# Kernel optimization log

Measured on AMD Instinct MI355X. Metric: run time of the kernel, lower is better.

The kernel has to match this reference:

```python
import jax, jax.numpy as jnp
import numpy as np

N_HEAD = 16


def _rope_cache(T, head_dim):
    half = head_dim // 2
    inv_freq = 1.0 / (10000.0 ** (jnp.arange(half, dtype=jnp.float32) / half))
    t = jnp.arange(T, dtype=jnp.float32)
    freqs = jnp.einsum('i,j->ij', t, inv_freq)            # (T, half)
    cos = jnp.repeat(jnp.cos(freqs), 2, axis=-1)          # (T, head_dim)
    sin = jnp.repeat(jnp.sin(freqs), 2, axis=-1)
    return cos, sin


def _apply_rope(x, cos, sin):
    # x: (B, H, T, D); cos/sin: (T, D)
    x1 = x[..., ::2]
    x2 = x[..., 1::2]
    x_rot = jnp.stack([-x2, x1], axis=-1).reshape(x.shape)
    return x * cos[None, None] + x_rot * sin[None, None]


def setup_inputs() -> dict:
    key = jax.random.key(0)
    k1, k2, k3 = jax.random.split(key, 3)
    B, T, C = 2, 2048, 1024
    x = jax.random.normal(k1, (B, T, C), dtype=jnp.float32)
    Wqkv = jax.random.normal(k2, (C, 3 * C), dtype=jnp.float32) * 0.02
    Wo = jax.random.normal(k3, (C, C), dtype=jnp.float32) * 0.02
    bo = jnp.zeros((C,), dtype=jnp.float32)
    return {"x": x, "Wqkv": Wqkv, "Wo": Wo, "bo": bo}


def reference(x, Wqkv, Wo, bo):
    B, T, C = x.shape
    H = N_HEAD
    D = C // H
    scale = D ** -0.5

    qkv = x @ Wqkv                                        # (B, T, 3C)
    qkv = qkv.reshape(B, T, 3, H, D).transpose(2, 0, 3, 1, 4)  # (3, B, H, T, D)
    q, k, v = qkv[0], qkv[1], qkv[2]

    cos, sin = _rope_cache(T, D)
    q = _apply_rope(q, cos, sin)
    k = _apply_rope(k, cos, sin)

    att = jnp.einsum('bhqd,bhkd->bhqk', q, k) * scale     # (B, H, T, T)
    causal = jnp.tril(jnp.ones((T, T), dtype=bool))
    att = jnp.where(causal[None, None], att, -jnp.inf)
    att = jax.nn.softmax(att, axis=-1)                    # dropout is identity in eval

    out = jnp.einsum('bhqk,bhkd->bhqd', att, v)           # (B, H, T, D)
    out = out.transpose(0, 2, 1, 3).reshape(B, T, C)
    return out @ Wo + bo
```

## Files before the change

### kernel.cpp

```cpp
#include <hip/hip_runtime.h>

typedef __attribute__((ext_vector_type(8))) short bf16x8;
typedef __attribute__((ext_vector_type(4))) float f32x4;
typedef __attribute__((ext_vector_type(4))) unsigned uint32x4;

#define MFMA32(a, b, c) __builtin_amdgcn_mfma_f32_16x16x32_bf16((a), (b), (c), 0, 0, 0)

__device__ __forceinline__ unsigned short f2bf(float f) {
  unsigned u = __builtin_bit_cast(unsigned, f);
  u += 0x7fffu + ((u >> 16) & 1u);
  return (unsigned short)(u >> 16);
}
__device__ __forceinline__ unsigned pack2(float a, float b) {
  return (unsigned)f2bf(a) | ((unsigned)f2bf(b) << 16);
}
__device__ __forceinline__ unsigned pack2t(float lo, float hi) {
  return __builtin_amdgcn_perm(__builtin_bit_cast(unsigned, hi),
                               __builtin_bit_cast(unsigned, lo), 0x07060302u);
}
__device__ __forceinline__ void gl_lds16(const unsigned short* g, unsigned short* l) {
  __builtin_amdgcn_global_load_lds(
      (const __attribute__((address_space(1))) unsigned int*)(g),
      (__attribute__((address_space(3))) unsigned int*)(l), 16, 0, 0);
}

#define QSCALE 0.18033688011112042f

__global__ __launch_bounds__(256) void prep_kernel(
    const float* __restrict__ x, const float* __restrict__ Wqkv,
    const float* __restrict__ Wo, unsigned short* __restrict__ xb,
    unsigned short* __restrict__ wqt, unsigned short* __restrict__ wot) {
  __shared__ unsigned short Tl[64][72];
  const int bid = blockIdx.x, tid = threadIdx.x;
  if (bid < 2048) {
    int i = (bid * 256 + tid) * 8;
    float4 a = *(const float4*)(x + i);
    float4 b = *(const float4*)(x + i + 4);
    uint4 w;
    w.x = pack2(a.x, a.y); w.y = pack2(a.z, a.w);
    w.z = pack2(b.x, b.y); w.w = pack2(b.z, b.w);
    *(uint4*)(xb + i) = w;
  } else {
    const float* src;
    unsigned short* dst;
    int N, kt, nt;
    if (bid < 2816) {
      int r = bid - 2048;
      src = Wqkv; dst = wqt; N = 3072;
      nt = (r % 48) * 64; kt = (r / 48) * 64;
    } else {
      int r = bid - 2816;
      src = Wo; dst = wot; N = 1024;
      nt = (r & 15) * 64; kt = (r >> 4) * 64;
    }
    const int rr = tid >> 2, cs = (tid & 3) * 16;
    const float* sp = src + (kt + rr) * N + nt + cs;
    uint4 w0, w1;
    {
      float4 a = *(const float4*)(sp), b = *(const float4*)(sp + 4);
      float4 c = *(const float4*)(sp + 8), d = *(const float4*)(sp + 12);
      w0.x = pack2(a.x, a.y); w0.y = pack2(a.z, a.w);
      w0.z = pack2(b.x, b.y); w0.w = pack2(b.z, b.w);
      w1.x = pack2(c.x, c.y); w1.y = pack2(c.z, c.w);
      w1.z = pack2(d.x, d.y); w1.w = pack2(d.z, d.w);
    }
    *(uint4*)(&Tl[rr][cs]) = w0;
    *(uint4*)(&Tl[rr][cs + 8]) = w1;
    __syncthreads();
    unsigned short tmp[16];
#pragma unroll
    for (int i = 0; i < 16; i++) tmp[i] = Tl[cs + i][rr];
    unsigned short* dp = dst + (nt + rr) * 1024 + kt + cs;
    *(uint4*)(dp) = *(const uint4*)(&tmp[0]);
    *(uint4*)(dp + 8) = *(const uint4*)(&tmp[8]);
  }
}

__global__ __launch_bounds__(256, 6) void qkv_rope_kernel(
    const unsigned short* __restrict__ xb, const unsigned short* __restrict__ wt,
    unsigned short* __restrict__ qws, unsigned short* __restrict__ kws,
    unsigned short* __restrict__ vws) {
  __shared__ unsigned short Al[2 * 64 * 32];
  __shared__ unsigned short Bl[2 * 128 * 32];

  const int tid = threadIdx.x;
  const int lane = tid & 63, wid = tid >> 6;
  const int quad = lane >> 4, col = lane & 15;
  const int wm = (wid >> 1) * 32, wn = (wid & 1) * 64;
  const int n0 = blockIdx.x * 128, m0 = blockIdx.y * 64;

  f32x4 acc[2][4] = {};
  const int srA = wid * 16 + (lane >> 2);
  const int srB = wid * 32 + (lane >> 2);
  const int gseg = ((lane & 3) ^ ((lane >> 3) & 3)) * 8;
  const int fsg = (quad ^ ((col >> 1) & 3)) * 8;

  for (int k0 = 0; k0 < 1024; k0 += 64) {
#pragma unroll
    for (int c = 0; c < 2; c++) {
      const int kc = k0 + c * 32;
      gl_lds16(xb + (m0 + srA) * 1024 + kc + gseg, Al + c * 2048 + (wid * 16) * 32);
      gl_lds16(wt + (n0 + srB) * 1024 + kc + gseg, Bl + c * 4096 + (wid * 32) * 32);
      gl_lds16(wt + (n0 + srB + 16) * 1024 + kc + gseg,
               Bl + c * 4096 + (wid * 32 + 16) * 32);
    }
    __syncthreads();

#pragma unroll
    for (int c = 0; c < 2; c++) {
      bf16x8 af[2], bfr[4];
#pragma unroll
      for (int i = 0; i < 2; i++)
        af[i] = *(const bf16x8*)(&Al[c * 2048 + (wm + i * 16 + col) * 32 + fsg]);
#pragma unroll
      for (int j = 0; j < 4; j++)
        bfr[j] = *(const bf16x8*)(&Bl[c * 4096 + (wn + j * 16 + col) * 32 + fsg]);
#pragma unroll
      for (int i = 0; i < 2; i++)
#pragma unroll
        for (int j = 0; j < 4; j++)
          acc[i][j] = MFMA32(af[i], bfr[j], acc[i][j]);
    }
    __syncthreads();
  }

#pragma unroll
  for (int i = 0; i < 2; i++) {
#pragma unroll
    for (int j = 0; j < 4; j++) {
      const int nbase = n0 + wn + j * 16;
      const int region = nbase >> 10;
#pragma unroll
      for (int r = 0; r < 4; r++) {
        int m = m0 + wm + i * 16 + quad * 4 + r;
        int n = nbase + col;
        float val = acc[i][j][r];
        int nn = n & 1023, h = nn >> 6, d = nn & 63, b = m >> 11, t = m & 2047;
        if (region < 2) {
          float other = __shfl_xor(val, 1);
          float invf = __expf(-(float)(d >> 1) * 0.28782313662425572f);
          float ang = (float)t * invf;
          float sn, cs;
          __sincosf(ang, &sn, &cs);
          float rot = (d & 1) ? other : -other;
          val = fmaf(val, cs, rot * sn);
        }
        int bh = (b << 4) + h;
        if (region == 0) {
          qws[(bh * 2048 + t) * 64 + d] = f2bf(val * QSCALE);
        } else if (region == 1) {
          kws[(bh * 2048 + t) * 64 + d] = f2bf(val);
        } else {
          int tl = t & 31, g = t >> 5;
          int qd = (tl & 15) >> 2;
          int jj = (tl & 3) + ((tl & 16) ? 4 : 0);
          int tp = g * 32 + qd * 8 + jj;
          vws[(bh * 64 + d) * 2048 + tp] = f2bf(val);
        }
      }
    }
  }
}

__global__ __launch_bounds__(256, 4) void attn_kernel(
    const unsigned short* __restrict__ qws, const unsigned short* __restrict__ kws,
    const unsigned short* __restrict__ vws, unsigned short* __restrict__ aws) {
  __shared__ unsigned short Kl[2][64 * 64];
  __shared__ unsigned short Vl[2][64 * 64];

  const int tid = threadIdx.x;
  const int lane = tid & 63, wid = tid >> 6;
  const int quad = lane >> 4, col = lane & 15;
  const int bh = blockIdx.x;
  const unsigned short* qb = qws + bh * (2048 * 64);
  const unsigned short* kb = kws + bh * (2048 * 64);
  const unsigned short* vb = vws + bh * (64 * 2048);
  const int b = bh >> 4, h = bh & 15;

  const int sro = wid * 16 + (lane >> 3);
  const int sgs = ((lane & 7) ^ ((lane >> 3) & 7)) * 8;
  const int sA = (quad ^ (col & 7)) * 8;

  const int q0blk = (31 - (int)blockIdx.y) * 64;
  const int qt = q0blk + wid * 16;
  const int qi = qt + col;
  const int qi_max = qt + 15;
  const int kend = q0blk + 64;

  bf16x8 qf0 = *(const bf16x8*)(qb + (qt + col) * 64 + quad * 8);
  bf16x8 qf1 = *(const bf16x8*)(qb + (qt + col) * 64 + 32 + quad * 8);

  f32x4 o[4] = {};
  float lsum = 0.f;

  for (int k0 = 0; k0 < kend; k0 += 128) {
    const int nsub = (kend - k0 > 64) ? 2 : 1;
    for (int u = 0; u < nsub; u++) {
      const int kb0 = k0 + u * 64;
      gl_lds16(kb + (kb0 + sro) * 64 + sgs, Kl[u] + (wid * 16) * 64);
      gl_lds16(kb + (kb0 + sro + 8) * 64 + sgs, Kl[u] + (wid * 16 + 8) * 64);
      gl_lds16(vb + sro * 2048 + kb0 + sgs, Vl[u] + (wid * 16) * 64);
      gl_lds16(vb + (sro + 8) * 2048 + kb0 + sgs, Vl[u] + (wid * 16 + 8) * 64);
    }
    __syncthreads();

    for (int u = 0; u < nsub; u++) {
      const int kb0 = k0 + u * 64;
      if (kb0 > qi_max) break;
      const int smax = min(4, ((qi_max - kb0) >> 4) + 1);
      const bool diag = (kb0 + 64 > qt);
      float p[16];
#pragma unroll
      for (int s = 0; s < 4; s++) {
        if (s < smax) {
          bf16x8 kfa = *(const bf16x8*)(&Kl[u][(s * 16 + col) * 64 + sA]);
          bf16x8 kfb = *(const bf16x8*)(&Kl[u][(s * 16 + col) * 64 + (sA ^ 32)]);
          f32x4 z = {0.f, 0.f, 0.f, 0.f};
          z = MFMA32(kfa, qf0, z);
          z = MFMA32(kfb, qf1, z);
          if (diag) {
#pragma unroll
            for (int r = 0; r < 4; r++)
              if (kb0 + s * 16 + quad * 4 + r > qi) z[r] = -1e30f;
          }
#pragma unroll
          for (int r = 0; r < 4; r++) {
            float e = exp2f(z[r]);
            p[s * 4 + r] = e;
            lsum += e;
          }
        } else {
#pragma unroll
          for (int r = 0; r < 4; r++) p[s * 4 + r] = 0.f;
        }
      }
      uint32x4 u0;
      u0[0] = pack2t(p[0], p[1]);   u0[1] = pack2t(p[2], p[3]);
      u0[2] = pack2t(p[4], p[5]);   u0[3] = pack2t(p[6], p[7]);
      bf16x8 pf0 = __builtin_bit_cast(bf16x8, u0);
#pragma unroll
      for (int dt = 0; dt < 4; dt++) {
        bf16x8 vfa = *(const bf16x8*)(&Vl[u][(dt * 16 + col) * 64 + sA]);
        o[dt] = MFMA32(vfa, pf0, o[dt]);
      }
      if (smax > 2) {
        uint32x4 u1;
        u1[0] = pack2t(p[8], p[9]);   u1[1] = pack2t(p[10], p[11]);
        u1[2] = pack2t(p[12], p[13]); u1[3] = pack2t(p[14], p[15]);
        bf16x8 pf1 = __builtin_bit_cast(bf16x8, u1);
#pragma unroll
        for (int dt = 0; dt < 4; dt++) {
          bf16x8 vfb = *(const bf16x8*)(&Vl[u][(dt * 16 + col) * 64 + (sA ^ 32)]);
          o[dt] = MFMA32(vfb, pf1, o[dt]);
        }
      }
    }
    __syncthreads();
  }

  lsum += __shfl_xor(lsum, 16);
  lsum += __shfl_xor(lsum, 32);
  float inv = 1.0f / lsum;
#pragma unroll
  for (int dt = 0; dt < 4; dt++)
#pragma unroll
    for (int r = 0; r < 4; r++) {
      int d = dt * 16 + quad * 4 + r;
      aws[(b * 2048 + qt + col) * 1024 + h * 64 + d] = f2bf(o[dt][r] * inv);
    }
}

__global__ __launch_bounds__(256) void out_proj_kernel(
    const unsigned short* __restrict__ attn, const unsigned short* __restrict__ wot,
    const float* __restrict__ bo, float* __restrict__ out) {
  __shared__ unsigned short Al[2 * 64 * 32];
  __shared__ unsigned short Bl[2 * 128 * 32];

  const int tid = threadIdx.x;
  const int lane = tid & 63, wid = tid >> 6;
  const int quad = lane >> 4, col = lane & 15;
  const int wm = (wid >> 1) * 32, wn = (wid & 1) * 64;
  const int n0 = blockIdx.x * 128, m0 = blockIdx.y * 64;

  f32x4 acc[2][4] = {};
  const int sr = lane >> 2;
  const int gseg = ((lane & 3) ^ ((lane >> 3) & 3)) * 8;
  const int fsg = (quad ^ ((col >> 1) & 3)) * 8;

  for (int k0 = 0; k0 < 1024; k0 += 64) {
#pragma unroll
    for (int c = 0; c < 2; c++) {
      const int kc = k0 + c * 32;
      gl_lds16(attn + (m0 + wid * 16 + sr) * 1024 + kc + gseg,
               Al + c * 2048 + (wid * 16) * 32);
      gl_lds16(wot + (n0 + wid * 32 + sr) * 1024 + kc + gseg,
               Bl + c * 4096 + (wid * 32) * 32);
      gl_lds16(wot + (n0 + wid * 32 + 16 + sr) * 1024 + kc + gseg,
               Bl + c * 4096 + (wid * 32 + 16) * 32);
    }
    __syncthreads();

#pragma unroll
    for (int c = 0; c < 2; c++) {
      bf16x8 af[2], bfr[4];
#pragma unroll
      for (int i = 0; i < 2; i++)
        af[i] = *(const bf16x8*)(&Al[c * 2048 + (wm + i * 16 + col) * 32 + fsg]);
#pragma unroll
      for (int j = 0; j < 4; j++)
        bfr[j] = *(const bf16x8*)(&Bl[c * 4096 + (wn + j * 16 + col) * 32 + fsg]);
#pragma unroll
      for (int i = 0; i < 2; i++)
#pragma unroll
        for (int j = 0; j < 4; j++)
          acc[i][j] = MFMA32(af[i], bfr[j], acc[i][j]);
    }
    __syncthreads();
  }

#pragma unroll
  for (int i = 0; i < 2; i++)
#pragma unroll
    for (int j = 0; j < 4; j++)
#pragma unroll
      for (int r = 0; r < 4; r++) {
        int m = m0 + wm + i * 16 + quad * 4 + r;
        int n = n0 + wn + j * 16 + col;
        out[m * 1024 + n] = acc[i][j][r] + bo[n];
      }
}

extern "C" void kernel_launch(void* const* d_in, const int* in_sizes, int n_in,
                              void* d_out, int out_size, void* d_ws, size_t ws_size,
                              hipStream_t stream) {
  const float* x = (const float*)d_in[0];
  const float* Wqkv = (const float*)d_in[1];
  const float* Wo = (const float*)d_in[2];
  const float* bo = (const float*)d_in[3];
  float* out = (float*)d_out;

  unsigned short* qws = (unsigned short*)d_ws;
  unsigned short* kws = qws + 4194304;
  unsigned short* vws = kws + 4194304;
  unsigned short* xb  = vws + 4194304;
  unsigned short* aws = xb;
  unsigned short* wqt = xb + 4194304;
  unsigned short* wot = wqt + 3145728;

  prep_kernel<<<3072, 256, 0, stream>>>(x, Wqkv, Wo, xb, wqt, wot);
  qkv_rope_kernel<<<dim3(24, 64), 256, 0, stream>>>(xb, wqt, qws, kws, vws);
  attn_kernel<<<dim3(32, 32), 256, 0, stream>>>(qws, kws, vws, aws);
  out_proj_kernel<<<dim3(8, 64), 256, 0, stream>>>(aws, wot, bo, out);
}
```

Measured before the change: 185.6 us.

## Double-buffer LDS tiles with one barrier per iteration in all three kernels

The QKV GEMM, attention and output-projection kernels now use ping-pong LDS buffers. The next K-slice (or K/V tile) is issued with global_load_lds right after the barrier, so the copy overlaps the MFMA work on the current buffer, and the trailing __syncthreads per iteration is removed. Attention now steps one 64-key tile per iteration instead of loading two and then computing both. In exchange, LDS use per block doubles and the launch-bounds occupancy hint for the GEMMs drops to 3 blocks. Because the compiler waits for all outstanding loads at each barrier, the overlap is limited to one compute phase.

Measured after the change: 199.3 us. 1.07x slower.

```diff
diff --git a/kernel.cpp b/kernel.cpp
--- a/kernel.cpp
+++ b/kernel.cpp
@@ -76,12 +76,12 @@
   }
 }
 
-__global__ __launch_bounds__(256, 6) void qkv_rope_kernel(
+__global__ __launch_bounds__(256, 3) void qkv_rope_kernel(
     const unsigned short* __restrict__ xb, const unsigned short* __restrict__ wt,
     unsigned short* __restrict__ qws, unsigned short* __restrict__ kws,
     unsigned short* __restrict__ vws) {
-  __shared__ unsigned short Al[2 * 64 * 32];
-  __shared__ unsigned short Bl[2 * 128 * 32];
+  __shared__ unsigned short Al[2][2 * 64 * 32];
+  __shared__ unsigned short Bl[2][2 * 128 * 32];
 
   const int tid = threadIdx.x;
   const int lane = tid & 63, wid = tid >> 6;
@@ -95,33 +95,37 @@
   const int gseg = ((lane & 3) ^ ((lane >> 3) & 3)) * 8;
   const int fsg = (quad ^ ((col >> 1) & 3)) * 8;
 
-  for (int k0 = 0; k0 < 1024; k0 += 64) {
+  auto stage = [&](int buf, int k0) {
 #pragma unroll
     for (int c = 0; c < 2; c++) {
       const int kc = k0 + c * 32;
-      gl_lds16(xb + (m0 + srA) * 1024 + kc + gseg, Al + c * 2048 + (wid * 16) * 32);
-      gl_lds16(wt + (n0 + srB) * 1024 + kc + gseg, Bl + c * 4096 + (wid * 32) * 32);
+      gl_lds16(xb + (m0 + srA) * 1024 + kc + gseg, &Al[buf][c * 2048 + (wid * 16) * 32]);
+      gl_lds16(wt + (n0 + srB) * 1024 + kc + gseg, &Bl[buf][c * 4096 + (wid * 32) * 32]);
       gl_lds16(wt + (n0 + srB + 16) * 1024 + kc + gseg,
-               Bl + c * 4096 + (wid * 32 + 16) * 32);
-    }
+               &Bl[buf][c * 4096 + (wid * 32 + 16) * 32]);
+    }
+  };
+
+  stage(0, 0);
+  for (int it = 0; it < 16; it++) {
     __syncthreads();
-
+    if (it + 1 < 16) stage((it + 1) & 1, (it + 1) * 64);
+    const int buf = it & 1;
 #pragma unroll
     for (int c = 0; c < 2; c++) {
       bf16x8 af[2], bfr[4];
 #pragma unroll
       for (int i = 0; i < 2; i++)
-        af[i] = *(const bf16x8*)(&Al[c * 2048 + (wm + i * 16 + col) * 32 + fsg]);
+        af[i] = *(const bf16x8*)(&Al[buf][c * 2048 + (wm + i * 16 + col) * 32 + fsg]);
 #pragma unroll
       for (int j = 0; j < 4; j++)
-        bfr[j] = *(const bf16x8*)(&Bl[c * 4096 + (wn + j * 16 + col) * 32 + fsg]);
+        bfr[j] = *(const bf16x8*)(&Bl[buf][c * 4096 + (wn + j * 16 + col) * 32 + fsg]);
 #pragma unroll
       for (int i = 0; i < 2; i++)
 #pragma unroll
         for (int j = 0; j < 4; j++)
           acc[i][j] = MFMA32(af[i], bfr[j], acc[i][j]);
     }
-    __syncthreads();
   }
 
 #pragma unroll
@@ -185,7 +189,7 @@
   const int qt = q0blk + wid * 16;
   const int qi = qt + col;
   const int qi_max = qt + 15;
-  const int kend = q0blk + 64;
+  const int ntiles = (q0blk >> 6) + 1;
 
   bf16x8 qf0 = *(const bf16x8*)(qb + (qt + col) * 64 + quad * 8);
   bf16x8 qf1 = *(const bf16x8*)(qb + (qt + col) * 64 + 32 + quad * 8);
@@ -193,69 +197,66 @@
   f32x4 o[4] = {};
   float lsum = 0.f;
 
-  for (int k0 = 0; k0 < kend; k0 += 128) {
-    const int nsub = (kend - k0 > 64) ? 2 : 1;
-    for (int u = 0; u < nsub; u++) {
-      const int kb0 = k0 + u * 64;
-      gl_lds16(kb + (kb0 + sro) * 64 + sgs, Kl[u] + (wid * 16) * 64);
-      gl_lds16(kb + (kb0 + sro + 8) * 64 + sgs, Kl[u] + (wid * 16 + 8) * 64);
-      gl_lds16(vb + sro * 2048 + kb0 + sgs, Vl[u] + (wid * 16) * 64);
-      gl_lds16(vb + (sro + 8) * 2048 + kb0 + sgs, Vl[u] + (wid * 16 + 8) * 64);
-    }
+  auto stage = [&](int buf, int kb0) {
+    gl_lds16(kb + (kb0 + sro) * 64 + sgs, &Kl[buf][(wid * 16) * 64]);
+    gl_lds16(kb + (kb0 + sro + 8) * 64 + sgs, &Kl[buf][(wid * 16 + 8) * 64]);
+    gl_lds16(vb + sro * 2048 + kb0 + sgs, &Vl[buf][(wid * 16) * 64]);
+    gl_lds16(vb + (sro + 8) * 2048 + kb0 + sgs, &Vl[buf][(wid * 16 + 8) * 64]);
+  };
+
+  stage(0, 0);
+  for (int ti = 0; ti < ntiles; ti++) {
     __syncthreads();
-
-    for (int u = 0; u < nsub; u++) {
-      const int kb0 = k0 + u * 64;
-      if (kb0 > qi_max) break;
-      const int smax = min(4, ((qi_max - kb0) >> 4) + 1);
-      const bool diag = (kb0 + 64 > qt);
-      float p[16];
-#pragma unroll
-      for (int s = 0; s < 4; s++) {
-        if (s < smax) {
-          bf16x8 kfa = *(const bf16x8*)(&Kl[u][(s * 16 + col) * 64 + sA]);
-          bf16x8 kfb = *(const bf16x8*)(&Kl[u][(s * 16 + col) * 64 + (sA ^ 32)]);
-          f32x4 z = {0.f, 0.f, 0.f, 0.f};
-          z = MFMA32(kfa, qf0, z);
-          z = MFMA32(kfb, qf1, z);
-          if (diag) {
-#pragma unroll
-            for (int r = 0; r < 4; r++)
-              if (kb0 + s * 16 + quad * 4 + r > qi) z[r] = -1e30f;
-          }
-#pragma unroll
-          for (int r = 0; r < 4; r++) {
-            float e = exp2f(z[r]);
-            p[s * 4 + r] = e;
-            lsum += e;
-          }
-        } else {
-#pragma unroll
-          for (int r = 0; r < 4; r++) p[s * 4 + r] = 0.f;
+    if (ti + 1 < ntiles) stage((ti + 1) & 1, (ti + 1) * 64);
+    const int u = ti & 1;
+    const int kb0 = ti * 64;
+    const int smax = min(4, ((qi_max - kb0) >> 4) + 1);
+    const bool diag = (kb0 + 64 > qt);
+    float p[16];
+#pragma unroll
+    for (int s = 0; s < 4; s++) {
+      if (s < smax) {
+        bf16x8 kfa = *(const bf16x8*)(&Kl[u][(s * 16 + col) * 64 + sA]);
+        bf16x8 kfb = *(const bf16x8*)(&Kl[u][(s * 16 + col) * 64 + (sA ^ 32)]);
+        f32x4 z = {0.f, 0.f, 0.f, 0.f};
+        z = MFMA32(kfa, qf0, z);
+        z = MFMA32(kfb, qf1, z);
+        if (diag) {
+#pragma unroll
+          for (int r = 0; r < 4; r++)
+            if (kb0 + s * 16 + quad * 4 + r > qi) z[r] = -1e30f;
         }
+#pragma unroll
+        for (int r = 0; r < 4; r++) {
+          float e = exp2f(z[r]);
+          p[s * 4 + r] = e;
+          lsum += e;
+        }
+      } else {
+#pragma unroll
+        for (int r = 0; r < 4; r++) p[s * 4 + r] = 0.f;
       }
-      uint32x4 u0;
-      u0[0] = pack2t(p[0], p[1]);   u0[1] = pack2t(p[2], p[3]);
-      u0[2] = pack2t(p[4], p[5]);   u0[3] = pack2t(p[6], p[7]);
-      bf16x8 pf0 = __builtin_bit_cast(bf16x8, u0);
+    }
+    uint32x4 u0;
+    u0[0] = pack2t(p[0], p[1]);   u0[1] = pack2t(p[2], p[3]);
+    u0[2] = pack2t(p[4], p[5]);   u0[3] = pack2t(p[6], p[7]);
+    bf16x8 pf0 = __builtin_bit_cast(bf16x8, u0);
+#pragma unroll
+    for (int dt = 0; dt < 4; dt++) {
+      bf16x8 vfa = *(const bf16x8*)(&Vl[u][(dt * 16 + col) * 64 + sA]);
+      o[dt] = MFMA32(vfa, pf0, o[dt]);
+    }
+    if (smax > 2) {
+      uint32x4 u1;
+      u1[0] = pack2t(p[8], p[9]);   u1[1] = pack2t(p[10], p[11]);
+      u1[2] = pack2t(p[12], p[13]); u1[3] = pack2t(p[14], p[15]);
+      bf16x8 pf1 = __builtin_bit_cast(bf16x8, u1);
 #pragma unroll
       for (int dt = 0; dt < 4; dt++) {
-        bf16x8 vfa = *(const bf16x8*)(&Vl[u][(dt * 16 + col) * 64 + sA]);
-        o[dt] = MFMA32(vfa, pf0, o[dt]);
+        bf16x8 vfb = *(const bf16x8*)(&Vl[u][(dt * 16 + col) * 64 + (sA ^ 32)]);
+        o[dt] = MFMA32(vfb, pf1, o[dt]);
       }
-      if (smax > 2) {
-        uint32x4 u1;
-        u1[0] = pack2t(p[8], p[9]);   u1[1] = pack2t(p[10], p[11]);
-        u1[2] = pack2t(p[12], p[13]); u1[3] = pack2t(p[14], p[15]);
-        bf16x8 pf1 = __builtin_bit_cast(bf16x8, u1);
-#pragma unroll
-        for (int dt = 0; dt < 4; dt++) {
-          bf16x8 vfb = *(const bf16x8*)(&Vl[u][(dt * 16 + col) * 64 + (sA ^ 32)]);
-          o[dt] = MFMA32(vfb, pf1, o[dt]);
-        }
-      }
-    }
-    __syncthreads();
+    }
   }
 
   lsum += __shfl_xor(lsum, 16);
@@ -270,11 +271,11 @@
     }
 }
 
-__global__ __launch_bounds__(256) void out_proj_kernel(
+__global__ __launch_bounds__(256, 3) void out_proj_kernel(
     const unsigned short* __restrict__ attn, const unsigned short* __restrict__ wot,
     const float* __restrict__ bo, float* __restrict__ out) {
-  __shared__ unsigned short Al[2 * 64 * 32];
-  __shared__ unsigned short Bl[2 * 128 * 32];
+  __shared__ unsigned short Al[2][2 * 64 * 32];
+  __shared__ unsigned short Bl[2][2 * 128 * 32];
 
   const int tid = threadIdx.x;
   const int lane = tid & 63, wid = tid >> 6;
@@ -287,35 +288,39 @@
   const int gseg = ((lane & 3) ^ ((lane >> 3) & 3)) * 8;
   const int fsg = (quad ^ ((col >> 1) & 3)) * 8;
 
-  for (int k0 = 0; k0 < 1024; k0 += 64) {
+  auto stage = [&](int buf, int k0) {
 #pragma unroll
     for (int c = 0; c < 2; c++) {
       const int kc = k0 + c * 32;
       gl_lds16(attn + (m0 + wid * 16 + sr) * 1024 + kc + gseg,
-               Al + c * 2048 + (wid * 16) * 32);
+               &Al[buf][c * 2048 + (wid * 16) * 32]);
       gl_lds16(wot + (n0 + wid * 32 + sr) * 1024 + kc + gseg,
-               Bl + c * 4096 + (wid * 32) * 32);
+               &Bl[buf][c * 4096 + (wid * 32) * 32]);
       gl_lds16(wot + (n0 + wid * 32 + 16 + sr) * 1024 + kc + gseg,
-               Bl + c * 4096 + (wid * 32 + 16) * 32);
-    }
+               &Bl[buf][c * 4096 + (wid * 32 + 16) * 32]);
+    }
+  };
+
+  stage(0, 0);
+  for (int it = 0; it < 16; it++) {
     __syncthreads();
-
+    if (it + 1 < 16) stage((it + 1) & 1, (it + 1) * 64);
+    const int buf = it & 1;
 #pragma unroll
     for (int c = 0; c < 2; c++) {
       bf16x8 af[2], bfr[4];
 #pragma unroll
       for (int i = 0; i < 2; i++)
-        af[i] = *(const bf16x8*)(&Al[c * 2048 + (wm + i * 16 + col) * 32 + fsg]);
+        af[i] = *(const bf16x8*)(&Al[buf][c * 2048 + (wm + i * 16 + col) * 32 + fsg]);
 #pragma unroll
       for (int j = 0; j < 4; j++)
-        bfr[j] = *(const bf16x8*)(&Bl[c * 4096 + (wn + j * 16 + col) * 32 + fsg]);
+        bfr[j] = *(const bf16x8*)(&Bl[buf][c * 4096 + (wn + j * 16 + col) * 32 + fsg]);
 #pragma unroll
       for (int i = 0; i < 2; i++)
 #pragma unroll
         for (int j = 0; j < 4; j++)
           acc[i][j] = MFMA32(af[i], bfr[j], acc[i][j]);
     }
-    __syncthreads();
   }
 
 #pragma unroll
```
